# Kernel optimization log

Hardware: AMD Instinct MI355X
Metric: run time of the kernel (lower is better)

Reference implementation:

```python
import jax, jax.numpy as jnp
import numpy as np

TEMPERATURE = 0.07
EPS = 1e-12  # F.normalize eps


def _l2_normalize(x):
    # matches torch F.normalize(dim=1): x / max(||x||, eps)
    n = jnp.linalg.norm(x, axis=1, keepdims=True)
    return x / jnp.maximum(n, EPS)


def setup_inputs() -> dict:
    key = jax.random.key(0)
    k1, k2 = jax.random.split(key)
    N, Z = 4096, 256
    z1 = jax.random.normal(k1, (N, Z), dtype=jnp.float32)
    z2 = jax.random.normal(k2, (N, Z), dtype=jnp.float32)
    return {"z1": z1, "z2": z2}


def reference(z1, z2):
    N = z1.shape[0]
    z1n = _l2_normalize(z1)
    z2n = _l2_normalize(z2)
    reps = jnp.concatenate([z1n, z2n], axis=0)          # [2N, Z]
    sim = reps @ reps.T                                  # cosine sim (rows unit-norm)
    # positives: sim[i, i+N] for i<N and sim[i, i-N] for i>=N
    pos = jnp.concatenate([jnp.diagonal(sim, offset=N),
                           jnp.diagonal(sim, offset=-N)])  # [2N]
    # The row logits are {positive} U {all sims except self and positive},
    # i.e. all entries except the self-similarity diagonal.
    inv_t = 1.0 / TEMPERATURE
    twoN = 2 * N
    diag_mask = jnp.eye(twoN, dtype=bool)
    logits = jnp.where(diag_mask, -jnp.inf, sim * inv_t)   # [2N, 2N]
    lse = jax.nn.logsumexp(logits, axis=1)                 # [2N]
    # cross_entropy with label at the positive: -pos/T + lse, sum / 2N
    loss = jnp.mean(lse - pos * inv_t)
    return loss
```

## Files before the change

### kernel.cpp

```cpp
#include <hip/hip_runtime.h>
#include <hip/hip_bf16.h>

#define N_ROWS 4096
#define TWO_N  8192
#define ZDIM   256
#define INV_T  (1.0f/0.07f)
#define EXP_SCALE (INV_T * 1.44269504088896340736f)

typedef __attribute__((ext_vector_type(8))) short bf16x8;
typedef __attribute__((ext_vector_type(4))) float f32x4;

__device__ __forceinline__ void async_load16(const void* g, void* lds_uniform_base) {
  __builtin_amdgcn_global_load_lds(
      (const __attribute__((address_space(1))) void*)g,
      (__attribute__((address_space(3))) void*)lds_uniform_base, 16, 0, 0);
}

__global__ __launch_bounds__(256) void normalize_kernel(
    const float* __restrict__ z1, const float* __restrict__ z2,
    __hip_bfloat16* __restrict__ reps, float* __restrict__ pos,
    float* __restrict__ out) {
  const int b = blockIdx.x;
  const int t = threadIdx.x;
  const float x1 = z1[b * ZDIM + t];
  const float x2 = z2[b * ZDIM + t];
  float s1 = x1 * x1, s2 = x2 * x2, s3 = x1 * x2;
  #pragma unroll
  for (int m = 1; m < 64; m <<= 1) {
    s1 += __shfl_xor(s1, m, 64);
    s2 += __shfl_xor(s2, m, 64);
    s3 += __shfl_xor(s3, m, 64);
  }
  __shared__ float red[3][4];
  const int w = t >> 6, l = t & 63;
  if (l == 0) { red[0][w] = s1; red[1][w] = s2; red[2][w] = s3; }
  __syncthreads();
  const float n1 = red[0][0] + red[0][1] + red[0][2] + red[0][3];
  const float n2 = red[1][0] + red[1][1] + red[1][2] + red[1][3];
  const float dt = red[2][0] + red[2][1] + red[2][2] + red[2][3];
  const float inv1 = 1.0f / fmaxf(sqrtf(n1), 1e-12f);
  const float inv2 = 1.0f / fmaxf(sqrtf(n2), 1e-12f);
  reps[b * ZDIM + t]            = __float2bfloat16(x1 * inv1);
  reps[(b + N_ROWS) * ZDIM + t] = __float2bfloat16(x2 * inv2);
  if (t == 0) {
    pos[b] = dt * inv1 * inv2;
    if (b == 0) out[0] = INV_T;
  }
}

__global__ __launch_bounds__(256, 2) void simsum_kernel(
    const __hip_bfloat16* __restrict__ reps,
    float* __restrict__ rowscratch,
    float* __restrict__ colscratch) {
  __shared__ __align__(16) __hip_bfloat16 Alds[128 * 256];
  __shared__ __align__(16) __hip_bfloat16 Blds[128 * 64];

  const int tid  = threadIdx.x;
  const int lane = tid & 63;
  const int wave = tid >> 6;
  const int wm = wave >> 1, wn = wave & 1;
  const int quad = lane >> 4;
  const int l16  = lane & 15;
  const int itile = blockIdx.x;
  const int chunk = blockIdx.y;
  const int rowBase = itile * 128;
  const char* gbase = (const char*)reps;

  #pragma unroll
  for (int p = 0; p < 16; ++p) {
    const int cbase = p * 256 + (wave << 6);
    const int c = cbase + lane;
    const int row = c >> 5;
    const int ch = (c & 31) ^ (row & 7);
    const int gofs = ((rowBase + row) * ZDIM + ch * 8) * 2;
    async_load16(gbase + gofs, (char*)Alds + cbase * 16);
  }
  __syncthreads();

  const int nd = (chunk == 0) ? ((itile < 32) ? 5 : 4) : 4;

  float rowpart[16];
  #pragma unroll
  for (int i = 0; i < 16; ++i) rowpart[i] = 0.0f;

  const f32x4 zero4 = {0.0f, 0.0f, 0.0f, 0.0f};
  float* colred = (float*)Blds;

  for (int td = 0; td < nd; ++td) {
    const int d = (chunk == 0) ? ((td == 4) ? 32 : td) : (chunk * 4 + td);
    const int jtile = (itile + d) & 63;
    const int colBase = jtile * 128;
    const bool diag = (d == 0);

    f32x4 acc[4][4];
    #pragma unroll
    for (int mi = 0; mi < 4; ++mi)
      #pragma unroll
      for (int ni = 0; ni < 4; ++ni) acc[mi][ni] = zero4;

    for (int kc = 0; kc < 4; ++kc) {
      if (!diag) {
        #pragma unroll
        for (int p = 0; p < 4; ++p) {
          const int cbase = p * 256 + (wave << 6);
          const int c = cbase + lane;
          const int row = c >> 3;
          const int ch = (c & 7) ^ (row & 7);
          const int gofs = ((colBase + row) * ZDIM + kc * 64 + ch * 8) * 2;
          async_load16(gbase + gofs, (char*)Blds + cbase * 16);
        }
        __syncthreads();
      }

      #pragma unroll
      for (int kk2 = 0; kk2 < 2; ++kk2) {
        bf16x8 afrag[4], bfrag[4];
        #pragma unroll
        for (int mi = 0; mi < 4; ++mi) {
          const int m = wm * 64 + mi * 16 + l16;
          const int ch = kc * 8 + kk2 * 4 + quad;
          afrag[mi] = *(const bf16x8*)((const char*)Alds + (m * 32 + (ch ^ (m & 7))) * 16);
        }
        #pragma unroll
        for (int ni = 0; ni < 4; ++ni) {
          const int n = wn * 64 + ni * 16 + l16;
          if (diag) {
            const int ch = kc * 8 + kk2 * 4 + quad;
            bfrag[ni] = *(const bf16x8*)((const char*)Alds + (n * 32 + (ch ^ (n & 7))) * 16);
          } else {
            const int ch = kk2 * 4 + quad;
            bfrag[ni] = *(const bf16x8*)((const char*)Blds + (n * 8 + (ch ^ (n & 7))) * 16);
          }
        }
        #pragma unroll
        for (int mi = 0; mi < 4; ++mi)
          #pragma unroll
          for (int ni = 0; ni < 4; ++ni)
            acc[mi][ni] = __builtin_amdgcn_mfma_f32_16x16x32_bf16(
                afrag[mi], bfrag[ni], acc[mi][ni], 0, 0, 0);
      }
      if (!diag) __syncthreads();
    }

    float colpart[4] = {0.0f, 0.0f, 0.0f, 0.0f};
    #pragma unroll
    for (int mi = 0; mi < 4; ++mi) {
      #pragma unroll
      for (int r = 0; r < 4; ++r) {
        const int grow = rowBase + wm * 64 + mi * 16 + quad * 4 + r;
        float s = 0.0f;
        #pragma unroll
        for (int ni = 0; ni < 4; ++ni) {
          const int gcol = colBase + wn * 64 + ni * 16 + l16;
          const float v = acc[mi][ni][r];
          const float e = exp2f((v - 1.0f) * EXP_SCALE);
          if (!diag || grow != gcol) s += e;
          colpart[ni] += e;
        }
        rowpart[mi * 4 + r] += s;
      }
    }
    if (!diag) {
      #pragma unroll
      for (int ni = 0; ni < 4; ++ni) {
        float v = colpart[ni];
        v += __shfl_xor(v, 16, 64);
        v += __shfl_xor(v, 32, 64);
        if (quad == 0) colred[wm * 128 + wn * 64 + ni * 16 + l16] = v;
      }
      __syncthreads();
      if (tid < 128) {
        const float v = colred[tid] + colred[128 + tid];
        colscratch[(jtile * 32 + (d - 1)) * 128 + tid] = v;
      }
      __syncthreads();
    }
  }

  #pragma unroll
  for (int i = 0; i < 16; ++i) {
    float v = rowpart[i];
    v += __shfl_xor(v, 1, 64);
    v += __shfl_xor(v, 2, 64);
    v += __shfl_xor(v, 4, 64);
    v += __shfl_xor(v, 8, 64);
    rowpart[i] = v;
  }
  float* rowred = (float*)Blds;
  __syncthreads();
  if (l16 == 0) {
    #pragma unroll
    for (int mi = 0; mi < 4; ++mi)
      #pragma unroll
      for (int r = 0; r < 4; ++r)
        rowred[wn * 128 + wm * 64 + mi * 16 + quad * 4 + r] = rowpart[mi * 4 + r];
  }
  __syncthreads();
  if (tid < 128)
    rowscratch[(itile * 8 + chunk) * 128 + tid] = rowred[tid] + rowred[128 + tid];
}

__global__ __launch_bounds__(256) void reduce_kernel(
    const float* __restrict__ rowscratch, const float* __restrict__ colscratch,
    const float* __restrict__ pos, float* __restrict__ out) {
  const int j = blockIdx.x;
  const int tid = threadIdx.x;
  float v = 0.0f;
  if (tid < 128) {
    float s = 0.0f;
    #pragma unroll
    for (int c = 0; c < 8; ++c) s += rowscratch[(j * 8 + c) * 128 + tid];
    const int ns = (j < 32) ? 31 : 32;
    for (int si = 0; si < ns; ++si) s += colscratch[(j * 32 + si) * 128 + tid];
    v = logf(s) * (1.0f / (float)TWO_N);
  } else if (tid < 192) {
    v = -pos[j * 64 + (tid - 128)] * (INV_T / (float)N_ROWS);
  }
  #pragma unroll
  for (int m = 1; m < 64; m <<= 1) v += __shfl_xor(v, m, 64);
  __shared__ float red[4];
  if ((tid & 63) == 0) red[tid >> 6] = v;
  __syncthreads();
  if (tid == 0) atomicAdd(out, red[0] + red[1] + red[2] + red[3]);
}

extern "C" void kernel_launch(void* const* d_in, const int* in_sizes, int n_in,
                              void* d_out, int out_size, void* d_ws, size_t ws_size,
                              hipStream_t stream) {
  const float* z1 = (const float*)d_in[0];
  const float* z2 = (const float*)d_in[1];
  char* ws = (char*)d_ws;
  __hip_bfloat16* reps = (__hip_bfloat16*)ws;
  size_t off = (size_t)TWO_N * ZDIM * 2;
  float* pos = (float*)(ws + off);        off += N_ROWS * 4;
  float* rowscratch = (float*)(ws + off); off += 64 * 8 * 128 * 4;
  float* colscratch = (float*)(ws + off); off += 64 * 32 * 128 * 4;

  normalize_kernel<<<N_ROWS, 256, 0, stream>>>(z1, z2, reps, pos, (float*)d_out);
  simsum_kernel<<<dim3(64, 8), 256, 0, stream>>>(reps, rowscratch, colscratch);
  reduce_kernel<<<64, 256, 0, stream>>>(rowscratch, colscratch, pos, (float*)d_out);
}
```

Measured before the change: 100.5 us.

## Load full-K B tiles at once and halve grid to 256 blocks

Each simsum block now loads the entire 128x256 B tile into LDS in one pass instead of four K-chunks, removing per-chunk barriers, and processes 8 tile diagonals instead of 4, so the grid shrinks to 64x4. Column reduction uses a double-buffered LDS array to drop one barrier per tile. LDS use grows to about 130KB, forcing one block per CU, and the grid of 256 blocks roughly matches the CU count but gives less latency hiding, since B loads are no longer overlapped with compute.

```diff
diff --git a/kernel.cpp b/kernel.cpp
--- a/kernel.cpp
+++ b/kernel.cpp
@@ -48,12 +48,13 @@
   }
 }
 
-__global__ __launch_bounds__(256, 2) void simsum_kernel(
+__global__ __launch_bounds__(256, 1) void simsum_kernel(
     const __hip_bfloat16* __restrict__ reps,
     float* __restrict__ rowscratch,
     float* __restrict__ colscratch) {
   __shared__ __align__(16) __hip_bfloat16 Alds[128 * 256];
-  __shared__ __align__(16) __hip_bfloat16 Blds[128 * 64];
+  __shared__ __align__(16) __hip_bfloat16 Blds[128 * 256];
+  __shared__ float colred[2][256];
 
   const int tid  = threadIdx.x;
   const int lane = tid & 63;
@@ -72,65 +73,61 @@
     const int c = cbase + lane;
     const int row = c >> 5;
     const int ch = (c & 31) ^ (row & 7);
-    const int gofs = ((rowBase + row) * ZDIM + ch * 8) * 2;
-    async_load16(gbase + gofs, (char*)Alds + cbase * 16);
-  }
-  __syncthreads();
-
-  const int nd = (chunk == 0) ? ((itile < 32) ? 5 : 4) : 4;
+    async_load16(gbase + ((rowBase + row) * ZDIM + ch * 8) * 2,
+                 (char*)Alds + cbase * 16);
+  }
+  __syncthreads();
+
+  const int nd = (chunk == 0) ? ((itile < 32) ? 9 : 8) : 8;
 
   float rowpart[16];
   #pragma unroll
   for (int i = 0; i < 16; ++i) rowpart[i] = 0.0f;
 
   const f32x4 zero4 = {0.0f, 0.0f, 0.0f, 0.0f};
-  float* colred = (float*)Blds;
 
   for (int td = 0; td < nd; ++td) {
-    const int d = (chunk == 0) ? ((td == 4) ? 32 : td) : (chunk * 4 + td);
+    const int d = (chunk == 0) ? ((td == 8) ? 32 : td) : (chunk * 8 + td);
     const int jtile = (itile + d) & 63;
     const int colBase = jtile * 128;
     const bool diag = (d == 0);
 
+    if (!diag) {
+      __syncthreads();
+      #pragma unroll
+      for (int p = 0; p < 16; ++p) {
+        const int cbase = p * 256 + (wave << 6);
+        const int c = cbase + lane;
+        const int row = c >> 5;
+        const int ch = (c & 31) ^ (row & 7);
+        async_load16(gbase + ((colBase + row) * ZDIM + ch * 8) * 2,
+                     (char*)Blds + cbase * 16);
+      }
+      __syncthreads();
+    }
+
     f32x4 acc[4][4];
     #pragma unroll
     for (int mi = 0; mi < 4; ++mi)
       #pragma unroll
       for (int ni = 0; ni < 4; ++ni) acc[mi][ni] = zero4;
 
+    #pragma unroll
     for (int kc = 0; kc < 4; ++kc) {
-      if (!diag) {
-        #pragma unroll
-        for (int p = 0; p < 4; ++p) {
-          const int cbase = p * 256 + (wave << 6);
-          const int c = cbase + lane;
-          const int row = c >> 3;
-          const int ch = (c & 7) ^ (row & 7);
-          const int gofs = ((colBase + row) * ZDIM + kc * 64 + ch * 8) * 2;
-          async_load16(gbase + gofs, (char*)Blds + cbase * 16);
-        }
-        __syncthreads();
-      }
-
       #pragma unroll
       for (int kk2 = 0; kk2 < 2; ++kk2) {
+        const int CH = kc * 8 + kk2 * 4 + quad;
         bf16x8 afrag[4], bfrag[4];
         #pragma unroll
         for (int mi = 0; mi < 4; ++mi) {
           const int m = wm * 64 + mi * 16 + l16;
-          const int ch = kc * 8 + kk2 * 4 + quad;
-          afrag[mi] = *(const bf16x8*)((const char*)Alds + (m * 32 + (ch ^ (m & 7))) * 16);
+          afrag[mi] = *(const bf16x8*)((const char*)Alds + (m * 32 + (CH ^ (m & 7))) * 16);
         }
         #pragma unroll
         for (int ni = 0; ni < 4; ++ni) {
           const int n = wn * 64 + ni * 16 + l16;
-          if (diag) {
-            const int ch = kc * 8 + kk2 * 4 + quad;
-            bfrag[ni] = *(const bf16x8*)((const char*)Alds + (n * 32 + (ch ^ (n & 7))) * 16);
-          } else {
-            const int ch = kk2 * 4 + quad;
-            bfrag[ni] = *(const bf16x8*)((const char*)Blds + (n * 8 + (ch ^ (n & 7))) * 16);
-          }
+          const char* src = diag ? (const char*)Alds : (const char*)Blds;
+          bfrag[ni] = *(const bf16x8*)(src + (n * 32 + (CH ^ (n & 7))) * 16);
         }
         #pragma unroll
         for (int mi = 0; mi < 4; ++mi)
@@ -139,7 +136,6 @@
             acc[mi][ni] = __builtin_amdgcn_mfma_f32_16x16x32_bf16(
                 afrag[mi], bfrag[ni], acc[mi][ni], 0, 0, 0);
       }
-      if (!diag) __syncthreads();
     }
 
     float colpart[4] = {0.0f, 0.0f, 0.0f, 0.0f};
@@ -166,14 +162,12 @@
         float v = colpart[ni];
         v += __shfl_xor(v, 16, 64);
         v += __shfl_xor(v, 32, 64);
-        if (quad == 0) colred[wm * 128 + wn * 64 + ni * 16 + l16] = v;
+        if (quad == 0) colred[td & 1][wm * 128 + wn * 64 + ni * 16 + l16] = v;
       }
       __syncthreads();
-      if (tid < 128) {
-        const float v = colred[tid] + colred[128 + tid];
-        colscratch[(jtile * 32 + (d - 1)) * 128 + tid] = v;
-      }
-      __syncthreads();
+      if (tid < 128)
+        colscratch[(jtile * 32 + (d - 1)) * 128 + tid] =
+            colred[td & 1][tid] + colred[td & 1][128 + tid];
     }
   }
 
@@ -186,18 +180,17 @@
     v += __shfl_xor(v, 8, 64);
     rowpart[i] = v;
   }
-  float* rowred = (float*)Blds;
   __syncthreads();
   if (l16 == 0) {
     #pragma unroll
     for (int mi = 0; mi < 4; ++mi)
       #pragma unroll
       for (int r = 0; r < 4; ++r)
-        rowred[wn * 128 + wm * 64 + mi * 16 + quad * 4 + r] = rowpart[mi * 4 + r];
+        colred[0][wn * 128 + wm * 64 + mi * 16 + quad * 4 + r] = rowpart[mi * 4 + r];
   }
   __syncthreads();
   if (tid < 128)
-    rowscratch[(itile * 8 + chunk) * 128 + tid] = rowred[tid] + rowred[128 + tid];
+    rowscratch[(itile * 4 + chunk) * 128 + tid] = colred[0][tid] + colred[0][128 + tid];
 }
 
 __global__ __launch_bounds__(256) void reduce_kernel(
@@ -209,7 +202,7 @@
   if (tid < 128) {
     float s = 0.0f;
     #pragma unroll
-    for (int c = 0; c < 8; ++c) s += rowscratch[(j * 8 + c) * 128 + tid];
+    for (int c = 0; c < 4; ++c) s += rowscratch[(j * 4 + c) * 128 + tid];
     const int ns = (j < 32) ? 31 : 32;
     for (int si = 0; si < ns; ++si) s += colscratch[(j * 32 + si) * 128 + tid];
     v = logf(s) * (1.0f / (float)TWO_N);
@@ -233,10 +226,10 @@
   __hip_bfloat16* reps = (__hip_bfloat16*)ws;
   size_t off = (size_t)TWO_N * ZDIM * 2;
   float* pos = (float*)(ws + off);        off += N_ROWS * 4;
-  float* rowscratch = (float*)(ws + off); off += 64 * 8 * 128 * 4;
+  float* rowscratch = (float*)(ws + off); off += 64 * 4 * 128 * 4;
   float* colscratch = (float*)(ws + off); off += 64 * 32 * 128 * 4;
 
   normalize_kernel<<<N_ROWS, 256, 0, stream>>>(z1, z2, reps, pos, (float*)d_out);
-  simsum_kernel<<<dim3(64, 8), 256, 0, stream>>>(reps, rowscratch, colscratch);
+  simsum_kernel<<<dim3(64, 4), 256, 0, stream>>>(reps, rowscratch, colscratch);
   reduce_kernel<<<64, 256, 0, stream>>>(rowscratch, colscratch, pos, (float*)d_out);
 }
```

Result: slower. 113.4 us (+12.8%).
